# Performance work log

Hardware: AMD Instinct MI355X
Metric: run time of the kernel (lower is better)

## Reference

```python
import jax, jax.numpy as jnp
import numpy as np

N_NODES = 100000
N_EDGES = 600000
N_GRAPHS = 512
DIM = 128
N_LAYERS = 3
N_CLASSES = 2
BN_EPS = 1e-5


def setup_inputs() -> dict:
    key = jax.random.key(0)
    ks = jax.random.split(key, 16)
    s = 1.0 / np.sqrt(DIM)
    inp = {
        "x": jax.random.normal(ks[0], (N_NODES, DIM), dtype=jnp.float32),
        "edge_index": jax.random.randint(ks[1], (2, N_EDGES), 0, N_NODES, dtype=jnp.int32),
        "batch": jnp.sort(jax.random.randint(ks[2], (N_NODES,), 0, N_GRAPHS, dtype=jnp.int32)),
        # GIN MLP params per layer: Linear -> BN -> Linear -> BN
        "W1": jax.random.uniform(ks[3], (N_LAYERS, DIM, DIM), jnp.float32, -s, s),
        "b1": jax.random.uniform(ks[4], (N_LAYERS, DIM), jnp.float32, -s, s),
        "g1": jnp.ones((N_LAYERS, DIM), jnp.float32),
        "bt1": jnp.zeros((N_LAYERS, DIM), jnp.float32),
        "W2": jax.random.uniform(ks[5], (N_LAYERS, DIM, DIM), jnp.float32, -s, s),
        "b2": jax.random.uniform(ks[6], (N_LAYERS, DIM), jnp.float32, -s, s),
        "g2": jnp.ones((N_LAYERS, DIM), jnp.float32),
        "bt2": jnp.zeros((N_LAYERS, DIM), jnp.float32),
        # outer BatchNorm per layer
        "go": jnp.ones((N_LAYERS, DIM), jnp.float32),
        "bo": jnp.zeros((N_LAYERS, DIM), jnp.float32),
        # final classifier
        "fcW": jax.random.uniform(ks[7], (DIM, N_CLASSES), jnp.float32, -s, s),
        "fcb": jax.random.uniform(ks[8], (N_CLASSES,), jnp.float32, -s, s),
    }
    return inp


def _bn(h, g, b):
    # training-mode BatchNorm1d over nodes (axis 0), biased variance
    m = jnp.mean(h, axis=0)
    v = jnp.var(h, axis=0)
    return (h - m) * jax.lax.rsqrt(v + BN_EPS) * g + b


def reference(x, edge_index, batch, W1, b1, g1, bt1, W2, b2, g2, bt2, go, bo, fcW, fcb):
    src, dst = edge_index[0], edge_index[1]
    h = x
    for i in range(N_LAYERS):
        # GIN aggregate: sum_{j in N(i)} x_j  + (1+eps)*x_i, eps=0
        agg = jax.ops.segment_sum(h[src], dst, num_segments=N_NODES)
        h = agg + h
        # GIN MLP: Linear -> BN -> Linear -> BN
        h = _bn(h @ W1[i] + b1[i], g1[i], bt1[i])
        h = _bn(h @ W2[i] + b2[i], g2[i], bt2[i])
        # outer BN + ReLU (dropout p=0 is a no-op)
        h = jax.nn.relu(_bn(h, go[i], bo[i]))
    node_embeddings = h
    # global mean pool per graph
    sums = jax.ops.segment_sum(node_embeddings, batch, num_segments=N_GRAPHS)
    counts = jax.ops.segment_sum(jnp.ones((N_NODES,), jnp.float32), batch, num_segments=N_GRAPHS)
    graph_embedding = sums / jnp.maximum(counts, 1.0)[:, None]
    out = graph_embedding @ fcW + fcb
    return (node_embeddings, graph_embedding, out)
```

## Files before the change

### kernel.cpp

```cpp
#include <hip/hip_runtime.h>

#define NN 100000
#define NE 600000
#define NG 512
#define D 128
#define NL 3
#define EPS 1e-5f

__global__ __launch_bounds__(256) void k_hist(const int* __restrict__ ei,
                                              int* __restrict__ deg) {
    int e = blockIdx.x * 256 + threadIdx.x;
    if (e < NE) atomicAdd(&deg[ei[NE + e]], 1);
}

__global__ __launch_bounds__(256) void k_scan1(const int* __restrict__ deg,
                                               int* __restrict__ excl,
                                               int* __restrict__ bsum) {
    __shared__ int s[256];
    int i = blockIdx.x * 256 + threadIdx.x;
    int v = (i < NN) ? deg[i] : 0;
    s[threadIdx.x] = v;
    __syncthreads();
    #pragma unroll
    for (int st = 1; st < 256; st <<= 1) {
        int t = (threadIdx.x >= st) ? s[threadIdx.x - st] : 0;
        __syncthreads();
        s[threadIdx.x] += t;
        __syncthreads();
    }
    if (i < NN) excl[i] = s[threadIdx.x] - v;
    if (threadIdx.x == 255) bsum[blockIdx.x] = s[255];
}

__global__ __launch_bounds__(512) void k_scan2(int* __restrict__ bsum, int nb) {
    __shared__ int s[512];
    int v = (threadIdx.x < nb) ? bsum[threadIdx.x] : 0;
    s[threadIdx.x] = v;
    __syncthreads();
    #pragma unroll
    for (int st = 1; st < 512; st <<= 1) {
        int t = (threadIdx.x >= st) ? s[threadIdx.x - st] : 0;
        __syncthreads();
        s[threadIdx.x] += t;
        __syncthreads();
    }
    if (threadIdx.x < nb) bsum[threadIdx.x] = s[threadIdx.x] - v;
}

__global__ __launch_bounds__(256) void k_scan3(const int* __restrict__ excl,
                                               const int* __restrict__ bsum,
                                               int* __restrict__ off,
                                               int* __restrict__ cur) {
    int i = blockIdx.x * 256 + threadIdx.x;
    if (i < NN) {
        int o = excl[i] + bsum[blockIdx.x];
        off[i] = o;
        cur[i] = o;
    }
    if (i == 0) off[NN] = NE;
}

__global__ __launch_bounds__(256) void k_fill(const int* __restrict__ ei,
                                              int* __restrict__ cur,
                                              int* __restrict__ srcs) {
    int e = blockIdx.x * 256 + threadIdx.x;
    if (e < NE) {
        int d = ei[NE + e];
        int p = atomicAdd(&cur[d], 1);
        srcs[p] = ei[e];
    }
}

__global__ __launch_bounds__(256) void k_gather(const float4* __restrict__ hin,
                                                const int* __restrict__ off,
                                                const int* __restrict__ srcs,
                                                float4* __restrict__ g) {
    int t = blockIdx.x * 256 + threadIdx.x;
    int n = t >> 5;
    if (n >= NN) return;
    int f4 = t & 31;
    int lo = off[n], hi = off[n + 1];
    float4 acc = hin[(long)n * 32 + f4];
    for (int e = lo; e < hi; ++e) {
        int s = srcs[e];
        float4 v = hin[(long)s * 32 + f4];
        acc.x += v.x; acc.y += v.y; acc.z += v.z; acc.w += v.w;
    }
    g[(long)n * 32 + f4] = acc;
}

__global__ __launch_bounds__(256) void k_gather_aff(const float4* __restrict__ yin,
                                                    const int* __restrict__ off,
                                                    const int* __restrict__ srcs,
                                                    const float* __restrict__ affA,
                                                    const float* __restrict__ affB,
                                                    float4* __restrict__ g) {
    int t = blockIdx.x * 256 + threadIdx.x;
    int n = t >> 5;
    if (n >= NN) return;
    int f4 = t & 31;
    float4 A = *(const float4*)(affA + f4 * 4);
    float4 B = *(const float4*)(affB + f4 * 4);
    int lo = off[n], hi = off[n + 1];
    float4 v = yin[(long)n * 32 + f4];
    float4 acc;
    acc.x = fmaxf(fmaf(v.x, A.x, B.x), 0.f);
    acc.y = fmaxf(fmaf(v.y, A.y, B.y), 0.f);
    acc.z = fmaxf(fmaf(v.z, A.z, B.z), 0.f);
    acc.w = fmaxf(fmaf(v.w, A.w, B.w), 0.f);
    for (int e = lo; e < hi; ++e) {
        int s = srcs[e];
        float4 u = yin[(long)s * 32 + f4];
        acc.x += fmaxf(fmaf(u.x, A.x, B.x), 0.f);
        acc.y += fmaxf(fmaf(u.y, A.y, B.y), 0.f);
        acc.z += fmaxf(fmaf(u.z, A.z, B.z), 0.f);
        acc.w += fmaxf(fmaf(u.w, A.w, B.w), 0.f);
    }
    g[(long)n * 32 + f4] = acc;
}

#define BM 64
#define BK 32
#define RST 65

__global__ __launch_bounds__(256, 5) void k_gemm(const float* __restrict__ A,
                                                 const float* __restrict__ W,
                                                 const float* __restrict__ bias,
                                                 float* __restrict__ C,
                                                 float* __restrict__ sum,
                                                 float* __restrict__ sq) {
    __shared__ float Ws[BK * 128];
    __shared__ float As[BK * RST];
    const int tid = threadIdx.x;
    const int ty = tid >> 4;
    const int tx = tid & 15;
    const long base = (long)blockIdx.x * BM;

    float acc[4][8];
    #pragma unroll
    for (int i = 0; i < 4; ++i)
        #pragma unroll
        for (int c = 0; c < 8; ++c) acc[i][c] = 0.f;

    for (int kc = 0; kc < 128; kc += BK) {
        #pragma unroll
        for (int j = 0; j < 4; ++j) {
            int e = tid + j * 256;
            int k = e >> 5, q = e & 31;
            int p = ((q & 1) << 4) + (q >> 1);
            float4 v = *(const float4*)(W + (long)(kc + k) * 128 + q * 4);
            *(float4*)(&Ws[k * 128 + p * 4]) = v;
        }
        #pragma unroll
        for (int j = 0; j < 2; ++j) {
            int e = tid + j * 256;
            int row = e >> 3, cq = e & 7;
            long gr = base + row;
            float4 v = make_float4(0.f, 0.f, 0.f, 0.f);
            if (gr < NN) v = *(const float4*)(A + gr * D + kc + cq * 4);
            As[(cq * 4 + 0) * RST + row] = v.x;
            As[(cq * 4 + 1) * RST + row] = v.y;
            As[(cq * 4 + 2) * RST + row] = v.z;
            As[(cq * 4 + 3) * RST + row] = v.w;
        }
        __syncthreads();
        #pragma unroll
        for (int k = 0; k < BK; ++k) {
            float4 a4 = *(const float4*)(&As[k * RST + ty * 4]);
            float4 w0 = *(const float4*)(&Ws[k * 128 + tx * 4]);
            float4 w1 = *(const float4*)(&Ws[k * 128 + 64 + tx * 4]);
            float av[4] = {a4.x, a4.y, a4.z, a4.w};
            float wv[8] = {w0.x, w0.y, w0.z, w0.w, w1.x, w1.y, w1.z, w1.w};
            #pragma unroll
            for (int i = 0; i < 4; ++i)
                #pragma unroll
                for (int c = 0; c < 8; ++c) acc[i][c] = fmaf(av[i], wv[c], acc[i][c]);
        }
        __syncthreads();
    }

    float4 b0 = *(const float4*)(bias + tx * 8);
    float4 b1 = *(const float4*)(bias + tx * 8 + 4);
    float bv[8] = {b0.x, b0.y, b0.z, b0.w, b1.x, b1.y, b1.z, b1.w};
    float csum[8], csq[8];
    #pragma unroll
    for (int c = 0; c < 8; ++c) { csum[c] = 0.f; csq[c] = 0.f; }
    #pragma unroll
    for (int i = 0; i < 4; ++i) {
        long gr = base + ty * 4 + i;
        if (gr < NN) {
            float o[8];
            #pragma unroll
            for (int c = 0; c < 8; ++c) {
                o[c] = acc[i][c] + bv[c];
                csum[c] += o[c];
                csq[c] += o[c] * o[c];
            }
            *(float4*)(C + gr * D + tx * 8) = make_float4(o[0], o[1], o[2], o[3]);
            *(float4*)(C + gr * D + tx * 8 + 4) = make_float4(o[4], o[5], o[6], o[7]);
        }
    }
    float* red = Ws;
    __syncthreads();
    *(float4*)(&red[ty * 128 + tx * 8]) = make_float4(csum[0], csum[1], csum[2], csum[3]);
    *(float4*)(&red[ty * 128 + tx * 8 + 4]) = make_float4(csum[4], csum[5], csum[6], csum[7]);
    *(float4*)(&red[2048 + ty * 128 + tx * 8]) = make_float4(csq[0], csq[1], csq[2], csq[3]);
    *(float4*)(&red[2048 + ty * 128 + tx * 8 + 4]) = make_float4(csq[4], csq[5], csq[6], csq[7]);
    __syncthreads();
    if (tid < 128) {
        float t = 0.f;
        #pragma unroll
        for (int j = 0; j < 16; ++j) t += red[j * 128 + tid];
        atomicAdd(sum + tid, t);
    } else {
        int col = tid - 128;
        float t = 0.f;
        #pragma unroll
        for (int j = 0; j < 16; ++j) t += red[2048 + j * 128 + col];
        atomicAdd(sq + col, t);
    }
}

__global__ __launch_bounds__(128) void k_fold(const float* __restrict__ W2,
                                              float* __restrict__ sum,
                                              float* __restrict__ sq,
                                              const float* __restrict__ g1,
                                              const float* __restrict__ bt1,
                                              float* __restrict__ W2s,
                                              float* __restrict__ biasF) {
    int k = blockIdx.x, j = threadIdx.x;
    float m = sum[k] * (1.f / NN);
    float v = sq[k] * (1.f / NN) - m * m;
    __syncthreads();
    if (j == 0) { sum[k] = 0.f; sq[k] = 0.f; }
    float a = g1[k] * rsqrtf(v + EPS);
    float c = bt1[k] - m * a;
    float w = W2[(long)k * 128 + j];
    W2s[(long)k * 128 + j] = a * w;
    atomicAdd(biasF + j, c * w);
}

__global__ void k_fin2(float* __restrict__ sum, float* __restrict__ sq,
                       const float* __restrict__ g2, const float* __restrict__ go,
                       const float* __restrict__ bo, float* __restrict__ affA,
                       float* __restrict__ affB) {
    int f = threadIdx.x;
    float m = sum[f] * (1.f / NN);
    float v = sq[f] * (1.f / NN) - m * m;
    sum[f] = 0.f;
    sq[f] = 0.f;
    float t = g2[f] * rsqrtf(v + EPS);
    float vo = t * t * v;
    float Aa = t * rsqrtf(vo + EPS) * go[f];
    affA[f] = Aa;
    affB[f] = bo[f] - m * Aa;
}

__global__ __launch_bounds__(256) void k_affine(const float4* __restrict__ Y,
                                                const float* __restrict__ affA,
                                                const float* __restrict__ affB,
                                                float4* __restrict__ o1) {
    const long n4 = (long)NN * 32;
    for (long i = (long)blockIdx.x * 256 + threadIdx.x; i < n4;
         i += (long)gridDim.x * 256) {
        int c4 = (int)(i & 31) * 4;
        float4 v = Y[i];
        float4 A = *(const float4*)(affA + c4);
        float4 B = *(const float4*)(affB + c4);
        float4 r;
        r.x = fmaxf(fmaf(v.x, A.x, B.x), 0.f);
        r.y = fmaxf(fmaf(v.y, A.y, B.y), 0.f);
        r.z = fmaxf(fmaf(v.z, A.z, B.z), 0.f);
        r.w = fmaxf(fmaf(v.w, A.w, B.w), 0.f);
        o1[i] = r;
    }
}

__device__ __forceinline__ int lower_bound_i(const int* __restrict__ a, int n, int v) {
    int lo = 0, hi = n;
    while (lo < hi) {
        int m = (lo + hi) >> 1;
        if (a[m] < v) lo = m + 1; else hi = m;
    }
    return lo;
}

__global__ __launch_bounds__(128) void k_pool(const float* __restrict__ h,
                                              const int* __restrict__ batch,
                                              const float* __restrict__ fcW,
                                              const float* __restrict__ fcb,
                                              float* __restrict__ ge,
                                              float* __restrict__ out) {
    __shared__ float r0[128], r1[128];
    int g = blockIdx.x, j = threadIdx.x;
    int lo = lower_bound_i(batch, NN, g);
    int hi = lower_bound_i(batch, NN, g + 1);
    float s = 0.f;
    for (int r = lo; r < hi; ++r) s += h[(long)r * D + j];
    int cnt = hi - lo;
    float mean = s / (float)(cnt > 0 ? cnt : 1);
    ge[(long)g * D + j] = mean;
    r0[j] = mean * fcW[j * 2 + 0];
    r1[j] = mean * fcW[j * 2 + 1];
    __syncthreads();
    for (int st = 64; st > 0; st >>= 1) {
        if (j < st) { r0[j] += r0[j + st]; r1[j] += r1[j + st]; }
        __syncthreads();
    }
    if (j == 0) {
        out[g * 2 + 0] = r0[0] + fcb[0];
        out[g * 2 + 1] = r1[0] + fcb[1];
    }
}

extern "C" void kernel_launch(void* const* d_in, const int* in_sizes, int n_in,
                              void* d_out, int out_size, void* d_ws, size_t ws_size,
                              hipStream_t stream) {
    const float* x   = (const float*)d_in[0];
    const int*   ei  = (const int*)d_in[1];
    const int*   bat = (const int*)d_in[2];
    const float* W1  = (const float*)d_in[3];
    const float* b1  = (const float*)d_in[4];
    const float* g1  = (const float*)d_in[5];
    const float* bt1 = (const float*)d_in[6];
    const float* W2  = (const float*)d_in[7];
    const float* b2  = (const float*)d_in[8];
    const float* g2  = (const float*)d_in[9];
    const float* go  = (const float*)d_in[11];
    const float* bo  = (const float*)d_in[12];
    const float* fcW = (const float*)d_in[13];
    const float* fcb = (const float*)d_in[14];

    const long ND = (long)NN * D;
    float* H = (float*)d_ws;
    float* G = H + ND;
    float* S = G + ND;
    float* sum   = S;
    float* sq    = S + 128;
    float* biasF = S + 512;
    float* affA  = S + 640;
    float* affB  = S + 768;
    float* W2s   = S + 1024;
    int*   off   = (int*)(S + 1024 + 16384);
    int*   srcs  = off + (NN + 1);

    float* nodeEmb = (float*)d_out;
    float* ge   = nodeEmb + ND;
    float* out2 = ge + (long)NG * D;
    float* Y = nodeEmb;

    int* deg  = (int*)nodeEmb;
    int* excl = deg + NN;
    int* cur  = excl + NN;
    int* bsum = cur + NN;

    const int edgeGrid = (NE + 255) / 256;
    const int nodeGrid = (NN + 255) / 256;
    const int gathGrid = (int)(((long)NN * 32 + 255) / 256);
    const int gemmGrid = (NN + BM - 1) / BM;

    hipMemsetAsync(deg, 0, NN * sizeof(int), stream);
    k_hist<<<edgeGrid, 256, 0, stream>>>(ei, deg);
    k_scan1<<<nodeGrid, 256, 0, stream>>>(deg, excl, bsum);
    k_scan2<<<1, 512, 0, stream>>>(bsum, nodeGrid);
    k_scan3<<<nodeGrid, 256, 0, stream>>>(excl, bsum, off, cur);
    k_fill<<<edgeGrid, 256, 0, stream>>>(ei, cur, srcs);

    hipMemsetAsync(sum, 0, 256 * sizeof(float), stream);

    for (int l = 0; l < NL; ++l) {
        if (l == 0)
            k_gather<<<gathGrid, 256, 0, stream>>>((const float4*)x, off, srcs,
                                                   (float4*)G);
        else
            k_gather_aff<<<gathGrid, 256, 0, stream>>>((const float4*)G, off, srcs,
                                                       affA, affB, (float4*)H);
        const float* gin = (l == 0) ? G : H;

        k_gemm<<<gemmGrid, 256, 0, stream>>>(gin, W1 + (long)l * D * D, b1 + l * D,
                                             Y, sum, sq);
        hipMemcpyAsync(biasF, b2 + (long)l * D, D * sizeof(float),
                       hipMemcpyDeviceToDevice, stream);
        k_fold<<<128, 128, 0, stream>>>(W2 + (long)l * D * D, sum, sq,
                                        g1 + l * D, bt1 + l * D, W2s, biasF);

        k_gemm<<<gemmGrid, 256, 0, stream>>>(Y, W2s, biasF, G, sum, sq);
        k_fin2<<<1, 128, 0, stream>>>(sum, sq, g2 + l * D, go + l * D, bo + l * D,
                                      affA, affB);
    }

    k_affine<<<4096, 256, 0, stream>>>((const float4*)G, affA, affB,
                                       (float4*)nodeEmb);
    k_pool<<<NG, 128, 0, stream>>>(nodeEmb, bat, fcW, fcb, ge, out2);
}
```

Measured before the change: 858.6 us.

## Fuse final affine+ReLU with mean-pool via atomics, precompute graph offsets

```diff
diff --git a/kernel.cpp b/kernel.cpp
--- a/kernel.cpp
+++ b/kernel.cpp
@@ -68,6 +68,28 @@
         int d = ei[NE + e];
         int p = atomicAdd(&cur[d], 1);
         srcs[p] = ei[e];
+    }
+}
+
+__global__ __launch_bounds__(256) void k_goff(const int* __restrict__ batch,
+                                              int* __restrict__ goff,
+                                              const float* __restrict__ b2all,
+                                              float* __restrict__ biasFall) {
+    int i = blockIdx.x * 256 + threadIdx.x;
+    if (blockIdx.x == 0) {
+        for (int j = threadIdx.x; j < NL * D; j += 256) biasFall[j] = b2all[j];
+    }
+    if (i == 0) {
+        int b0 = batch[0];
+        for (int g = 0; g <= b0; ++g) goff[g] = 0;
+    }
+    if (i < NN - 1) {
+        int b = batch[i], bn = batch[i + 1];
+        for (int g = b + 1; g <= bn; ++g) goff[g] = i + 1;
+    }
+    if (i == NN - 1) {
+        int b = batch[NN - 1];
+        for (int g = b + 1; g <= NG; ++g) goff[g] = NN;
     }
 }
 
@@ -256,49 +278,61 @@
     affB[f] = bo[f] - m * Aa;
 }
 
-__global__ __launch_bounds__(256) void k_affine(const float4* __restrict__ Y,
-                                                const float* __restrict__ affA,
-                                                const float* __restrict__ affB,
-                                                float4* __restrict__ o1) {
-    const long n4 = (long)NN * 32;
-    for (long i = (long)blockIdx.x * 256 + threadIdx.x; i < n4;
-         i += (long)gridDim.x * 256) {
-        int c4 = (int)(i & 31) * 4;
-        float4 v = Y[i];
-        float4 A = *(const float4*)(affA + c4);
-        float4 B = *(const float4*)(affB + c4);
-        float4 r;
-        r.x = fmaxf(fmaf(v.x, A.x, B.x), 0.f);
-        r.y = fmaxf(fmaf(v.y, A.y, B.y), 0.f);
-        r.z = fmaxf(fmaf(v.z, A.z, B.z), 0.f);
-        r.w = fmaxf(fmaf(v.w, A.w, B.w), 0.f);
-        o1[i] = r;
-    }
-}
-
-__device__ __forceinline__ int lower_bound_i(const int* __restrict__ a, int n, int v) {
-    int lo = 0, hi = n;
-    while (lo < hi) {
-        int m = (lo + hi) >> 1;
-        if (a[m] < v) lo = m + 1; else hi = m;
-    }
-    return lo;
-}
-
-__global__ __launch_bounds__(128) void k_pool(const float* __restrict__ h,
-                                              const int* __restrict__ batch,
-                                              const float* __restrict__ fcW,
-                                              const float* __restrict__ fcb,
-                                              float* __restrict__ ge,
-                                              float* __restrict__ out) {
+__global__ __launch_bounds__(256) void k_affine_pool(const float4* __restrict__ Y,
+                                                     const float* __restrict__ affA,
+                                                     const float* __restrict__ affB,
+                                                     const int* __restrict__ batch,
+                                                     float4* __restrict__ nodeEmb,
+                                                     float* __restrict__ gsum) {
+    int tid = threadIdx.x;
+    int f4 = tid & 31;
+    int rg = tid >> 5;
+    long base = (long)blockIdx.x * 64 + (long)rg * 8;
+    float4 A = *(const float4*)(affA + f4 * 4);
+    float4 B = *(const float4*)(affB + f4 * 4);
+    float4 run = make_float4(0.f, 0.f, 0.f, 0.f);
+    int curg = -1;
+    #pragma unroll
+    for (int i = 0; i < 8; ++i) {
+        long r = base + i;
+        if (r >= NN) break;
+        int g = batch[r];
+        float4 v = Y[r * 32 + f4];
+        float4 o;
+        o.x = fmaxf(fmaf(v.x, A.x, B.x), 0.f);
+        o.y = fmaxf(fmaf(v.y, A.y, B.y), 0.f);
+        o.z = fmaxf(fmaf(v.z, A.z, B.z), 0.f);
+        o.w = fmaxf(fmaf(v.w, A.w, B.w), 0.f);
+        nodeEmb[r * 32 + f4] = o;
+        if (g != curg) {
+            if (curg >= 0) {
+                float* p = gsum + (long)curg * D + f4 * 4;
+                atomicAdd(p + 0, run.x); atomicAdd(p + 1, run.y);
+                atomicAdd(p + 2, run.z); atomicAdd(p + 3, run.w);
+            }
+            curg = g;
+            run = o;
+        } else {
+            run.x += o.x; run.y += o.y; run.z += o.z; run.w += o.w;
+        }
+    }
+    if (curg >= 0) {
+        float* p = gsum + (long)curg * D + f4 * 4;
+        atomicAdd(p + 0, run.x); atomicAdd(p + 1, run.y);
+        atomicAdd(p + 2, run.z); atomicAdd(p + 3, run.w);
+    }
+}
+
+__global__ __launch_bounds__(128) void k_fc(const float* __restrict__ gsum,
+                                            const int* __restrict__ goff,
+                                            const float* __restrict__ fcW,
+                                            const float* __restrict__ fcb,
+                                            float* __restrict__ ge,
+                                            float* __restrict__ out) {
     __shared__ float r0[128], r1[128];
     int g = blockIdx.x, j = threadIdx.x;
-    int lo = lower_bound_i(batch, NN, g);
-    int hi = lower_bound_i(batch, NN, g + 1);
-    float s = 0.f;
-    for (int r = lo; r < hi; ++r) s += h[(long)r * D + j];
-    int cnt = hi - lo;
-    float mean = s / (float)(cnt > 0 ? cnt : 1);
+    int cnt = goff[g + 1] - goff[g];
+    float mean = gsum[(long)g * D + j] / (float)(cnt > 0 ? cnt : 1);
     ge[(long)g * D + j] = mean;
     r0[j] = mean * fcW[j * 2 + 0];
     r1[j] = mean * fcW[j * 2 + 1];
@@ -335,14 +369,16 @@
     float* H = (float*)d_ws;
     float* G = H + ND;
     float* S = G + ND;
-    float* sum   = S;
-    float* sq    = S + 128;
-    float* biasF = S + 512;
-    float* affA  = S + 640;
-    float* affB  = S + 768;
-    float* W2s   = S + 1024;
-    int*   off   = (int*)(S + 1024 + 16384);
-    int*   srcs  = off + (NN + 1);
+    float* sum      = S;
+    float* sq       = S + 128;
+    float* gsum     = S + 256;
+    float* biasFall = S + 65792;
+    float* affA     = S + 66176;
+    float* affB     = S + 66304;
+    float* W2s      = S + 66432;
+    int*   goff     = (int*)(S + 82816);
+    int*   off      = (int*)(S + 83840);
+    int*   srcs     = off + (NN + 1);
 
     float* nodeEmb = (float*)d_out;
     float* ge   = nodeEmb + ND;
@@ -358,6 +394,7 @@
     const int nodeGrid = (NN + 255) / 256;
     const int gathGrid = (int)(((long)NN * 32 + 255) / 256);
     const int gemmGrid = (NN + BM - 1) / BM;
+    const int apGrid   = (NN + 63) / 64;
 
     hipMemsetAsync(deg, 0, NN * sizeof(int), stream);
     k_hist<<<edgeGrid, 256, 0, stream>>>(ei, deg);
@@ -366,7 +403,8 @@
     k_scan3<<<nodeGrid, 256, 0, stream>>>(excl, bsum, off, cur);
     k_fill<<<edgeGrid, 256, 0, stream>>>(ei, cur, srcs);
 
-    hipMemsetAsync(sum, 0, 256 * sizeof(float), stream);
+    hipMemsetAsync(sum, 0, (256 + (long)NG * D) * sizeof(float), stream);
+    k_goff<<<nodeGrid, 256, 0, stream>>>(bat, goff, b2, biasFall);
 
     for (int l = 0; l < NL; ++l) {
         if (l == 0)
@@ -379,17 +417,17 @@
 
         k_gemm<<<gemmGrid, 256, 0, stream>>>(gin, W1 + (long)l * D * D, b1 + l * D,
                                              Y, sum, sq);
-        hipMemcpyAsync(biasF, b2 + (long)l * D, D * sizeof(float),
-                       hipMemcpyDeviceToDevice, stream);
         k_fold<<<128, 128, 0, stream>>>(W2 + (long)l * D * D, sum, sq,
-                                        g1 + l * D, bt1 + l * D, W2s, biasF);
-
-        k_gemm<<<gemmGrid, 256, 0, stream>>>(Y, W2s, biasF, G, sum, sq);
+                                        g1 + l * D, bt1 + l * D, W2s,
+                                        biasFall + (long)l * D);
+
+        k_gemm<<<gemmGrid, 256, 0, stream>>>(Y, W2s, biasFall + (long)l * D,
+                                             G, sum, sq);
         k_fin2<<<1, 128, 0, stream>>>(sum, sq, g2 + l * D, go + l * D, bo + l * D,
                                       affA, affB);
     }
 
-    k_affine<<<4096, 256, 0, stream>>>((const float4*)G, affA, affB,
-                                       (float4*)nodeEmb);
-    k_pool<<<NG, 128, 0, stream>>>(nodeEmb, bat, fcW, fcb, ge, out2);
-}
+    k_affine_pool<<<apGrid, 256, 0, stream>>>((const float4*)G, affA, affB, bat,
+                                              (float4*)nodeEmb, gsum);
+    k_fc<<<NG, 128, 0, stream>>>(gsum, goff, fcW, fcb, ge, out2);
+}
```

New measurement: 794.8 us. 1.08x faster.
